# Kernel optimization log

Hardware: AMD Instinct MI355X
Metric: run time of the kernel (lower is better)

Reference implementation:

```python
import jax, jax.numpy as jnp
import numpy as np

NUM_HEADS = 16
LN_EPS = 1e-5


def _transpose_qkv(X, num_heads):
    # Faithful to the repo's (buggy) transpose_qkv:
    # (B,S,D) -> (B,S,H,D/H) -> permute (B,H,S,D/H) -> reshape (B,S,D)
    B, S, D = X.shape
    X = X.reshape(B, S, num_heads, D // num_heads)
    X = jnp.transpose(X, (0, 2, 1, 3))
    return X.reshape(B, S, D)


def _layer_norm(x, w, b):
    mu = jnp.mean(x, axis=-1, keepdims=True)
    var = jnp.var(x, axis=-1, keepdims=True)
    return (x - mu) * jax.lax.rsqrt(var + LN_EPS) * w + b


def setup_inputs() -> dict:
    key = jax.random.key(0)
    ks = jax.random.split(key, 4)
    B, S, D = 4, 2048, 1024
    scale = 1.0 / np.sqrt(D)
    return {
        "src": jax.random.normal(ks[0], (B, S, D), dtype=jnp.float32),
        "W_q": jax.random.normal(ks[1], (D, D), dtype=jnp.float32) * scale,
        "W_k": jax.random.normal(ks[2], (D, D), dtype=jnp.float32) * scale,
        "W_v": jax.random.normal(ks[3], (D, D), dtype=jnp.float32) * scale,
        "ln1_w": jnp.ones((D,), dtype=jnp.float32),
        "ln1_b": jnp.zeros((D,), dtype=jnp.float32),
        "ln2_w": jnp.ones((D,), dtype=jnp.float32),
        "ln2_b": jnp.zeros((D,), dtype=jnp.float32),
    }


def reference(src, W_q, W_k, W_v, ln1_w, ln1_b, ln2_w, ln2_b):
    # W_* stored as (in, out): y = x @ W  (equivalent to torch Linear, bias=False)
    q = _transpose_qkv(src @ W_q, NUM_HEADS)  # (B,S,D)
    k = _transpose_qkv(src @ W_k, NUM_HEADS)
    v = _transpose_qkv(src @ W_v, NUM_HEADS)
    d = q.shape[-1]  # note: full hidden dim, per the buggy transpose_qkv
    scores = jnp.einsum("bqd,bkd->bqk", q, k) / jnp.sqrt(jnp.float32(d))
    a = jax.nn.softmax(scores, axis=-1)          # (B,S,S) attention weights
    att = jnp.einsum("bqk,bkd->bqd", a, v)       # (B,S,D)
    src2 = _layer_norm(att, ln1_w, ln1_b)        # norm1
    X = _layer_norm(src + src2, ln2_w, ln2_b)    # AddNorm (dropout=0 in eval)
    return (X, a)
```

## Files before the change

### kernel.cpp

```cpp
#include <hip/hip_runtime.h>

typedef _Float16 f16;
typedef __attribute__((ext_vector_type(2))) _Float16 f16x2;
typedef __attribute__((ext_vector_type(4))) _Float16 f16x4;
typedef __attribute__((ext_vector_type(8))) _Float16 f16x8;
typedef __attribute__((ext_vector_type(4))) float f32x4;

#define D_MODEL 1024
#define SEQ 2048
#define NBATCH 4
#define NROWS (NBATCH * SEQ)

__device__ __forceinline__ void gload16(const void* g, void* l) {
  __builtin_amdgcn_global_load_lds(
      (__attribute__((address_space(1))) void*)(void*)g,
      (__attribute__((address_space(3))) void*)l, 16, 0, 0);
}

#define BARF                                   \
  do {                                         \
    asm volatile("" ::: "memory");             \
    __builtin_amdgcn_s_barrier();              \
    asm volatile("" ::: "memory");             \
  } while (0)
#define PRIO1 __builtin_amdgcn_s_setprio(1)
#define PRIO0 __builtin_amdgcn_s_setprio(0)

template <int BN>
__device__ __forceinline__ void gemm8_core(
    const f16* aP0, const f16* aP1, const f16* aP2, const f16* aP3,
    const f16* bP0, const f16* bP1, const f16* bP2, const f16* bP3,
    int stepA, int stepB, int NT, f16* lds, f32x4* acc)
{
  constexpr int NJ = BN / 128;
  constexpr int NACC = 2 * NJ;
  constexpr int SLOT = 16384 + BN * 64;
  const int t = threadIdx.x, l = t & 63;
  const int w = t >> 6, wm = w >> 2, wn = w & 3;
  const int fr = l & 15, g0 = l >> 4;

  int aof[2][4][2], bof[2][NJ][2];
#pragma unroll
  for (int mh = 0; mh < 2; ++mh)
#pragma unroll
    for (int mi = 0; mi < 4; ++mi)
#pragma unroll
      for (int kh = 0; kh < 2; ++kh) {
        const int ra = wm * 128 + mh * 64 + mi * 16 + fr;
        aof[mh][mi][kh] = ra * 64 + (((g0 + kh * 4) ^ (ra & 7)) << 3);
      }
#pragma unroll
  for (int nh = 0; nh < 2; ++nh)
#pragma unroll
    for (int j = 0; j < NJ; ++j)
#pragma unroll
      for (int kh = 0; kh < 2; ++kh) {
        const int rb = (BN == 256) ? (wn * 64 + fr * 4 + nh * 2 + j)
                                   : (wn * 32 + fr * 2 + nh);
        bof[nh][j][kh] = rb * 64 + (((g0 + kh * 4) ^ ((rb >> 2) & 7)) << 3);
      }
#pragma unroll
  for (int i = 0; i < 8 * NACC; ++i) acc[i] = f32x4{0.f, 0.f, 0.f, 0.f};

  f16x8 fa[4][2];
  f16x8 fb[2][NJ][2];

#define STAGE_A(SL)                                  \
  {                                                  \
    f16* d = lds + (SL) * SLOT + t * 8;              \
    gload16(aP0, d);                                 \
    gload16(aP1, d + 4096);                          \
    gload16(aP2, d + 8192);                          \
    gload16(aP3, d + 12288);                         \
  }
#define STAGE_B(SL)                                  \
  {                                                  \
    f16* d = lds + (SL) * SLOT + 16384 + t * 8;      \
    gload16(bP0, d);                                 \
    gload16(bP1, d + 4096);                          \
    if constexpr (BN == 256) {                       \
      gload16(bP2, d + 8192);                        \
      gload16(bP3, d + 12288);                       \
    }                                                \
  }
#define ADVA { aP0 += stepA; aP1 += stepA; aP2 += stepA; aP3 += stepA; }
#define ADVB                                         \
  {                                                  \
    bP0 += stepB; bP1 += stepB;                      \
    if constexpr (BN == 256) { bP2 += stepB; bP3 += stepB; } \
  }
#define VMC                                                        \
  if constexpr (BN == 256) {                                       \
    asm volatile("s_waitcnt vmcnt(4)" ::: "memory");               \
  } else {                                                         \
    asm volatile("s_waitcnt vmcnt(2)" ::: "memory");               \
  }
#define LOAD_A(MH)                                   \
  _Pragma("unroll") for (int mi = 0; mi < 4; ++mi)   \
  _Pragma("unroll") for (int kh = 0; kh < 2; ++kh)   \
      fa[mi][kh] = *(const f16x8*)(LA + aof[MH][mi][kh]);
#define LOAD_B(NH)                                   \
  _Pragma("unroll") for (int j = 0; j < NJ; ++j)     \
  _Pragma("unroll") for (int kh = 0; kh < 2; ++kh)   \
      fb[NH][j][kh] = *(const f16x8*)(LBp + bof[NH][j][kh]);
#define MFMA_BLK(MH, NH)                                                    \
  _Pragma("unroll") for (int mi = 0; mi < 4; ++mi)                          \
  _Pragma("unroll") for (int j = 0; j < NJ; ++j)                            \
  _Pragma("unroll") for (int kh = 0; kh < 2; ++kh)                          \
      acc[((MH)*4 + mi) * NACC + (NH)*NJ + j] =                             \
          __builtin_amdgcn_mfma_f32_16x16x32_f16(                           \
              fa[mi][kh], fb[NH][j][kh],                                    \
              acc[((MH)*4 + mi) * NACC + (NH)*NJ + j], 0, 0, 0);

  (void)bP2; (void)bP3;
  STAGE_A(0); ADVA;
  STAGE_B(0); ADVB;
  STAGE_B(1); ADVB;
  VMC;
  BARF;

  for (int kt = 0; kt < NT; ++kt) {
    const int sl = kt & 1;
    const f16* LA = lds + sl * SLOT;
    const f16* LBp = LA + 16384;
    STAGE_A(sl ^ 1);
    if (kt + 2 < NT) ADVA;
    LOAD_A(0); LOAD_B(0); LOAD_B(1);
    PRIO1; MFMA_BLK(0, 0); MFMA_BLK(0, 1); PRIO0;
    BARF;
    LOAD_A(1);
    STAGE_B(sl);
    if (kt + 3 < NT) ADVB;
    VMC;
    PRIO1; MFMA_BLK(1, 0); MFMA_BLK(1, 1); PRIO0;
    BARF;
  }
#undef STAGE_A
#undef STAGE_B
#undef ADVA
#undef ADVB
#undef VMC
#undef LOAD_A
#undef LOAD_B
#undef MFMA_BLK
}

__global__ __launch_bounds__(512, 2) void k_qkv3(
    const f16* __restrict__ srch, const f16* __restrict__ wt,
    f16* __restrict__ qp, f16* __restrict__ kp, f16* __restrict__ vp)
{
  __shared__ f16 lds[2 * (16384 + 128 * 64)];
  const int t = threadIdx.x, l = t & 63;
  const int w = t >> 6, wm = w >> 2, wn = w & 3;
  const int fr = l & 15, g0 = l >> 4, c = t & 7;
  const int z = blockIdx.y >> 3, cb = blockIdx.y & 7;
  const f16 *aP[4], *bP[2];
#pragma unroll
  for (int i = 0; i < 4; ++i) {
    const int rl = i * 64 + (t >> 3);
    aP[i] = srch + (size_t)(blockIdx.x * 256 + rl) * 1024 + ((c ^ (rl & 7)) << 3);
  }
#pragma unroll
  for (int i = 0; i < 2; ++i) {
    const int rl = i * 64 + (t >> 3);
    bP[i] = wt + ((size_t)z << 20) + (size_t)(cb * 128 + rl) * 1024 +
            ((c ^ ((rl >> 2) & 7)) << 3);
  }
  f32x4 acc[16];
  gemm8_core<128>(aP[0], aP[1], aP[2], aP[3], bP[0], bP[1], bP[0], bP[0],
                  64, 64, 16, lds, acc);
  f16* dst = (z == 0) ? qp : (z == 1 ? kp : vp);
  const int col = cb * 128 + wn * 32 + fr * 2;
#pragma unroll
  for (int mi = 0; mi < 8; ++mi)
#pragma unroll
    for (int q = 0; q < 4; ++q) {
      const int row = blockIdx.x * 256 + wm * 128 + mi * 16 + g0 * 4 + q;
      f16x2 o = {(f16)acc[mi * 2 + 0][q], (f16)acc[mi * 2 + 1][q]};
      *(f16x2*)(dst + (size_t)row * 1024 + col) = o;
    }
}

__global__ __launch_bounds__(512, 2) void k_scores(
    const f16* __restrict__ qp, const f16* __restrict__ kp,
    f16* __restrict__ abf, float* __restrict__ sums)
{
  __shared__ f16 lds[2 * (16384 + 256 * 64)];
  const int t = threadIdx.x, l = t & 63;
  const int w = t >> 6, wm = w >> 2, wn = w & 3;
  const int fr = l & 15, g0 = l >> 4, c = t & 7;
  const int id = blockIdx.x;
  const int wg = ((id & 7) << 5) + (id >> 3);
  const int b = wg >> 6, by = (wg >> 3) & 7, bx = wg & 7;
  const f16* qb = qp + ((size_t)b << 21);
  const f16* kb = kp + ((size_t)b << 21);
  const f16 *aP[4], *bP[4];
#pragma unroll
  for (int i = 0; i < 4; ++i) {
    const int rl = i * 64 + (t >> 3);
    const int spA = bx * 256 + rl;
    aP[i] = qb + (size_t)((spA & 127) << 4) * 1024 + ((spA >> 7) << 6) +
            ((c ^ (rl & 7)) << 3);
    const int spB = by * 256 + rl;
    bP[i] = kb + (size_t)((spB & 127) << 4) * 1024 + ((spB >> 7) << 6) +
            ((c ^ ((rl >> 2) & 7)) << 3);
  }
  f32x4 acc[32];
  gemm8_core<256>(aP[0], aP[1], aP[2], aP[3], bP[0], bP[1], bP[2], bP[3],
                  1024, 1024, 16, lds, acc);
  f16* Cb = abf + ((size_t)b << 22);
  float* sums_b = sums + (b << 11);
  const int col = by * 256 + wn * 64 + fr * 4;
#pragma unroll
  for (int mi = 0; mi < 8; ++mi)
#pragma unroll
    for (int q = 0; q < 4; ++q) {
      const int row = bx * 256 + wm * 128 + mi * 16 + g0 * 4 + q;
      float e0 = __expf(acc[mi * 4 + 0][q] * 0.03125f);
      float e1 = __expf(acc[mi * 4 + 1][q] * 0.03125f);
      float e2 = __expf(acc[mi * 4 + 2][q] * 0.03125f);
      float e3 = __expf(acc[mi * 4 + 3][q] * 0.03125f);
      f16x4 o = {(f16)e0, (f16)e1, (f16)e2, (f16)e3};
      *(f16x4*)(Cb + (size_t)row * 2048 + col) = o;
      float p = e0 + e1 + e2 + e3;
      p += __shfl_xor(p, 1);
      p += __shfl_xor(p, 2);
      p += __shfl_xor(p, 4);
      p += __shfl_xor(p, 8);
      if (fr == 0) atomicAdd(&sums_b[row], p);
    }
}

__global__ __launch_bounds__(512, 2) void k_att(
    const f16* __restrict__ abf, const f16* __restrict__ vtT,
    const float* __restrict__ sums, f16* __restrict__ attb,
    float* __restrict__ Aout)
{
  __shared__ f16 lds[2 * (16384 + 128 * 64)];
  const int t = threadIdx.x, l = t & 63;
  const int w = t >> 6, wm = w >> 2, wn = w & 3;
  const int fr = l & 15, g0 = l >> 4, c = t & 7;
  const int id = blockIdx.x;
  const int wg = ((id & 7) << 5) + (id >> 3);
  const int b = wg >> 6, by = (wg >> 3) & 7, bx = wg & 7;
  const f16* ab = abf + ((size_t)b << 22);
  const f16* vb = vtT + ((size_t)b << 21);
  const f16 *aP[4], *bP[2];
#pragma unroll
  for (int i = 0; i < 4; ++i) {
    const int rl = i * 64 + (t >> 3);
    aP[i] = ab + (size_t)(bx * 256 + rl) * 2048 + ((c ^ (rl & 7)) << 3);
  }
#pragma unroll
  for (int i = 0; i < 2; ++i) {
    const int rl = i * 64 + (t >> 3);
    bP[i] = vb + (size_t)(by * 128 + rl) * 2048 +
            ((c ^ ((rl >> 2) & 7)) << 3);
  }
  f32x4 acc[16];
  gemm8_core<128>(aP[0], aP[1], aP[2], aP[3], bP[0], bP[1], bP[0], bP[0],
                  64, 64, 32, lds, acc);
  const float* sums_b = sums + (b << 11);
  f16* Cb = attb + ((size_t)b << 21);
  const int col = by * 128 + wn * 32 + fr * 2;
#pragma unroll
  for (int mi = 0; mi < 8; ++mi)
#pragma unroll
    for (int q = 0; q < 4; ++q) {
      const int row = bx * 256 + wm * 128 + mi * 16 + g0 * 4 + q;
      const float is = 1.0f / sums_b[row];
      f16x2 o = {(f16)(acc[mi * 2 + 0][q] * is), (f16)(acc[mi * 2 + 1][q] * is)};
      *(f16x2*)(Cb + (size_t)row * 1024 + col) = o;
    }
  float* Ab = Aout + ((size_t)b << 22);
#pragma unroll
  for (int i = 0; i < 16; ++i) {
    const int idx = t + i * 512;
    const int rr = idx >> 5;
    const int cg = (idx & 31) * 8;
    const int grow = bx * 256 + rr;
    const float is = 1.0f / sums_b[grow];
    f16x8 ev = *(const f16x8*)(ab + (size_t)grow * 2048 + by * 256 + cg);
    float4 o0 = {(float)ev[0] * is, (float)ev[1] * is,
                 (float)ev[2] * is, (float)ev[3] * is};
    float4 o1 = {(float)ev[4] * is, (float)ev[5] * is,
                 (float)ev[6] * is, (float)ev[7] * is};
    float* dst = Ab + (size_t)grow * 2048 + by * 256 + cg;
    *(float4*)dst = o0;
    *(float4*)(dst + 4) = o1;
  }
}

__global__ __launch_bounds__(256) void k_prep(
    const float* __restrict__ src, const float* __restrict__ w0,
    const float* __restrict__ w1, const float* __restrict__ w2,
    f16* __restrict__ srch, f16* __restrict__ wt)
{
  const int b = blockIdx.x, t = threadIdx.x;
  if (b < 4096) {
    const size_t i = (size_t)b * 256 + t;
    const float4* p = (const float4*)src;
    float4 v0 = p[2 * i], v1 = p[2 * i + 1];
    f16x8 o;
    o[0] = (f16)v0.x; o[1] = (f16)v0.y; o[2] = (f16)v0.z; o[3] = (f16)v0.w;
    o[4] = (f16)v1.x; o[5] = (f16)v1.y; o[6] = (f16)v1.z; o[7] = (f16)v1.w;
    *(f16x8*)(srch + 8 * i) = o;
    return;
  }
  const int id = b - 4096;
  const int z = id >> 8, rem = id & 255;
  const int bx = rem & 15, by = rem >> 4;
  const float* in = (z == 0) ? w0 : (z == 1 ? w1 : w2);
  f16* o = wt + ((size_t)z << 20);
  __shared__ f16 tile[64][65];
  const int rr = t >> 4, c4 = (t & 15) * 4;
  const int r0 = bx * 64, c0 = by * 64;
#pragma unroll
  for (int i = 0; i < 4; ++i) {
    float4 f = *(const float4*)(in + (size_t)(r0 + rr + 16 * i) * 1024 + c0 + c4);
    tile[rr + 16 * i][c4 + 0] = (f16)f.x;
    tile[rr + 16 * i][c4 + 1] = (f16)f.y;
    tile[rr + 16 * i][c4 + 2] = (f16)f.z;
    tile[rr + 16 * i][c4 + 3] = (f16)f.w;
  }
  __syncthreads();
#pragma unroll
  for (int i = 0; i < 4; ++i) {
    const int n = c0 + rr + 16 * i;
    f16* dst = o + (size_t)n * 1024 + r0 + c4;
    dst[0] = tile[c4 + 0][rr + 16 * i];
    dst[1] = tile[c4 + 1][rr + 16 * i];
    dst[2] = tile[c4 + 2][rr + 16 * i];
    dst[3] = tile[c4 + 3][rr + 16 * i];
  }
}

__global__ __launch_bounds__(256) void k_scrT(const f16* __restrict__ vp,
                                              f16* __restrict__ vtT,
                                              float* __restrict__ sums)
{
  const int t = threadIdx.x;
  if (blockIdx.x == 2048) {
    f32x4 z = {0.f, 0.f, 0.f, 0.f};
#pragma unroll
    for (int i = 0; i < 8; ++i)
      *(f32x4*)(sums + (size_t)(t * 8 + i * 2048) * 4 / 4 + 0) = z,
      ((f32x4*)sums)[t + i * 256] = z;
    return;
  }
  __shared__ f16 tile[64][68];
  const int id = blockIdx.x;
  const int sx = id & 31, sy = (id >> 5) & 15, bz = id >> 9;
  const int sp0 = sx * 64, dp0 = sy * 64;
  const int d6 = dp0 >> 6;
  const int jb = (sp0 >> 7) << 6;
  const int sbase = sp0 & 127;
  const f16* srcv = vp + ((size_t)bz << 21);
  f16* dstv = vtT + ((size_t)bz << 21);
#pragma unroll
  for (int p = 0; p < 2; ++p) {
    const int u = p * 32 + (t >> 3);
    const int s = ((sbase + u) << 4) | d6;
    const int cc = (t & 7) << 3;
    f16x8 v = *(const f16x8*)(srcv + (size_t)s * 1024 + jb + cc);
    *(f16x4*)&tile[u][cc]     = f16x4{v[0], v[1], v[2], v[3]};
    *(f16x4*)&tile[u][cc + 4] = f16x4{v[4], v[5], v[6], v[7]};
  }
  __syncthreads();
#pragma unroll
  for (int p = 0; p < 2; ++p) {
    const int cc = p * 32 + (t >> 3);
    const int v0 = (t & 7) << 3;
    f16x8 o;
#pragma unroll
    for (int j = 0; j < 8; ++j) o[j] = tile[v0 + j][cc];
    *(f16x8*)(dstv + (size_t)(dp0 + cc) * 2048 + sp0 + v0) = o;
  }
}

__global__ __launch_bounds__(256) void k_ln(
    const f16* __restrict__ attb, const float* __restrict__ src,
    const float* __restrict__ w1, const float* __restrict__ b1,
    const float* __restrict__ w2, const float* __restrict__ b2,
    float* __restrict__ out)
{
  const size_t base = (size_t)blockIdx.x * 1024;
  const int t = threadIdx.x, lane = t & 63, w = t >> 6;
  f16x4 a4 = ((const f16x4*)(attb + base))[t];
  float ax = (float)a4[0], ay = (float)a4[1], az = (float)a4[2], aw = (float)a4[3];
  float s = ax + ay + az + aw;
  float s2 = ax * ax + ay * ay + az * az + aw * aw;
#pragma unroll
  for (int off = 1; off < 64; off <<= 1) {
    s += __shfl_xor(s, off);
    s2 += __shfl_xor(s2, off);
  }
  __shared__ float red[16];
  if (lane == 0) { red[w] = s; red[4 + w] = s2; }
  __syncthreads();
  s = red[0] + red[1] + red[2] + red[3];
  s2 = red[4] + red[5] + red[6] + red[7];
  float mu = s * (1.0f / 1024.0f);
  float var = s2 * (1.0f / 1024.0f) - mu * mu;
  float rs = rsqrtf(var + 1e-5f);
  float4 W1 = ((const float4*)w1)[t], B1 = ((const float4*)b1)[t];
  float4 sv = ((const float4*)(src + base))[t];
  float y0 = sv.x + (ax - mu) * rs * W1.x + B1.x;
  float y1 = sv.y + (ay - mu) * rs * W1.y + B1.y;
  float y2 = sv.z + (az - mu) * rs * W1.z + B1.z;
  float y3 = sv.w + (aw - mu) * rs * W1.w + B1.w;
  s = y0 + y1 + y2 + y3;
  s2 = y0 * y0 + y1 * y1 + y2 * y2 + y3 * y3;
#pragma unroll
  for (int off = 1; off < 64; off <<= 1) {
    s += __shfl_xor(s, off);
    s2 += __shfl_xor(s2, off);
  }
  if (lane == 0) { red[8 + w] = s; red[12 + w] = s2; }
  __syncthreads();
  s = red[8] + red[9] + red[10] + red[11];
  s2 = red[12] + red[13] + red[14] + red[15];
  mu = s * (1.0f / 1024.0f);
  var = s2 * (1.0f / 1024.0f) - mu * mu;
  rs = rsqrtf(var + 1e-5f);
  float4 W2 = ((const float4*)w2)[t], B2 = ((const float4*)b2)[t];
  float4 o;
  o.x = (y0 - mu) * rs * W2.x + B2.x;
  o.y = (y1 - mu) * rs * W2.y + B2.y;
  o.z = (y2 - mu) * rs * W2.z + B2.z;
  o.w = (y3 - mu) * rs * W2.w + B2.w;
  ((float4*)(out + base))[t] = o;
}

extern "C" void kernel_launch(void* const* d_in, const int* in_sizes, int n_in,
                              void* d_out, int out_size, void* d_ws, size_t ws_size,
                              hipStream_t stream) {
  const float* src = (const float*)d_in[0];
  const float* Wq  = (const float*)d_in[1];
  const float* Wk  = (const float*)d_in[2];
  const float* Wv  = (const float*)d_in[3];
  const float* l1w = (const float*)d_in[4];
  const float* l1b = (const float*)d_in[5];
  const float* l2w = (const float*)d_in[6];
  const float* l2b = (const float*)d_in[7];
  float* Xout = (float*)d_out;
  float* Aout = Xout + (size_t)NROWS * D_MODEL;

  char* ws = (char*)d_ws;
  f16* srch = (f16*)ws;
  float* sums = (float*)ws;
  f16* wt   = (f16*)(ws + (16u << 20));
  f16* qp   = (f16*)(ws + (22u << 20));
  f16* kp   = (f16*)(ws + (38u << 20));
  f16* vp   = (f16*)(ws + (54u << 20));
  f16* vtT  = (f16*)(ws + (70u << 20));
  f16* abf  = (f16*)(ws + (86u << 20));
  f16* attb = (f16*)(ws + (118u << 20));

  k_prep<<<4864, 256, 0, stream>>>(src, Wq, Wk, Wv, srch, wt);
  k_qkv3<<<dim3(32, 24), 512, 0, stream>>>(srch, wt, qp, kp, vp);
  k_scrT<<<2049, 256, 0, stream>>>(vp, vtT, sums);
  k_scores<<<256, 512, 0, stream>>>(qp, kp, abf, sums);
  k_att<<<256, 512, 0, stream>>>(abf, vtT, sums, attb, Aout);
  k_ln<<<NROWS, 256, 0, stream>>>(attb, src, l1w, l1b, l2w, l2b, Xout);
}
```

Measured before the change: 193.2 us.

## Inline attention-V GEMM loop and fuse normalized A output writes from LDS fragments

Replaces the generic gemm8_core call in k_att with an inlined double-buffered loop that stages A and V tiles through LDS and interleaves MFMA halves with barriers. The fp32 attention-weight output is now written from the fragments already loaded for the MFMA, by the wn==0 waves when the k-tile falls in this block's column slice. This drops the separate epilogue that re-read the unnormalized fp16 scores from global memory. It also removes a redundant duplicate zeroing store in k_scrT. The cost is more register pressure and store work placed inside the main loop for some waves, which may unbalance them.

```diff
diff --git a/kernel.cpp b/kernel.cpp
--- a/kernel.cpp
+++ b/kernel.cpp
@@ -245,22 +245,132 @@
   const int b = wg >> 6, by = (wg >> 3) & 7, bx = wg & 7;
   const f16* ab = abf + ((size_t)b << 22);
   const f16* vb = vtT + ((size_t)b << 21);
-  const f16 *aP[4], *bP[2];
-#pragma unroll
-  for (int i = 0; i < 4; ++i) {
-    const int rl = i * 64 + (t >> 3);
-    aP[i] = ab + (size_t)(bx * 256 + rl) * 2048 + ((c ^ (rl & 7)) << 3);
-  }
-#pragma unroll
-  for (int i = 0; i < 2; ++i) {
-    const int rl = i * 64 + (t >> 3);
-    bP[i] = vb + (size_t)(by * 128 + rl) * 2048 +
-            ((c ^ ((rl >> 2) & 7)) << 3);
-  }
+  const float* sums_b = sums + (b << 11);
+  float* Ab = Aout + ((size_t)b << 22);
+
+  const f16 *aP0, *aP1, *aP2, *aP3, *bP0, *bP1;
+  {
+    const int rl0 = (t >> 3), rl1 = 64 + rl0, rl2 = 128 + rl0, rl3 = 192 + rl0;
+    aP0 = ab + (size_t)(bx * 256 + rl0) * 2048 + ((c ^ (rl0 & 7)) << 3);
+    aP1 = ab + (size_t)(bx * 256 + rl1) * 2048 + ((c ^ (rl1 & 7)) << 3);
+    aP2 = ab + (size_t)(bx * 256 + rl2) * 2048 + ((c ^ (rl2 & 7)) << 3);
+    aP3 = ab + (size_t)(bx * 256 + rl3) * 2048 + ((c ^ (rl3 & 7)) << 3);
+    bP0 = vb + (size_t)(by * 128 + rl0) * 2048 + ((c ^ ((rl0 >> 2) & 7)) << 3);
+    bP1 = vb + (size_t)(by * 128 + rl1) * 2048 + ((c ^ ((rl1 >> 2) & 7)) << 3);
+  }
+
+  int aof[2][4][2], bof[2][2];
+#pragma unroll
+  for (int mh = 0; mh < 2; ++mh)
+#pragma unroll
+    for (int mi = 0; mi < 4; ++mi)
+#pragma unroll
+      for (int kh = 0; kh < 2; ++kh) {
+        const int ra = wm * 128 + mh * 64 + mi * 16 + fr;
+        aof[mh][mi][kh] = ra * 64 + (((g0 + kh * 4) ^ (ra & 7)) << 3);
+      }
+#pragma unroll
+  for (int nh = 0; nh < 2; ++nh)
+#pragma unroll
+    for (int kh = 0; kh < 2; ++kh) {
+      const int rb = wn * 32 + fr * 2 + nh;
+      bof[nh][kh] = rb * 64 + (((g0 + kh * 4) ^ ((rb >> 2) & 7)) << 3);
+    }
+  float is8[2][4];
+#pragma unroll
+  for (int mh = 0; mh < 2; ++mh)
+#pragma unroll
+    for (int mi = 0; mi < 4; ++mi)
+      is8[mh][mi] = 1.0f / sums_b[bx * 256 + wm * 128 + mh * 64 + mi * 16 + fr];
+
   f32x4 acc[16];
-  gemm8_core<128>(aP[0], aP[1], aP[2], aP[3], bP[0], bP[1], bP[0], bP[0],
-                  64, 64, 32, lds, acc);
-  const float* sums_b = sums + (b << 11);
+#pragma unroll
+  for (int i = 0; i < 16; ++i) acc[i] = f32x4{0.f, 0.f, 0.f, 0.f};
+  f16x8 fa[4][2], fb[2][2];
+  constexpr int SLOT = 16384 + 8192;
+
+#define ASTG(SL)                                     \
+  {                                                  \
+    f16* d = lds + (SL) * SLOT + t * 8;              \
+    gload16(aP0, d);                                 \
+    gload16(aP1, d + 4096);                          \
+    gload16(aP2, d + 8192);                          \
+    gload16(aP3, d + 12288);                         \
+  }
+#define BSTG(SL)                                     \
+  {                                                  \
+    f16* d = lds + (SL) * SLOT + 16384 + t * 8;      \
+    gload16(bP0, d);                                 \
+    gload16(bP1, d + 4096);                          \
+  }
+#define AADV { aP0 += 64; aP1 += 64; aP2 += 64; aP3 += 64; }
+#define BADV { bP0 += 64; bP1 += 64; }
+#define VM2 asm volatile("s_waitcnt vmcnt(2)" ::: "memory")
+#define LDA_(MH)                                     \
+  _Pragma("unroll") for (int mi = 0; mi < 4; ++mi)   \
+  _Pragma("unroll") for (int kh = 0; kh < 2; ++kh)   \
+      fa[mi][kh] = *(const f16x8*)(LA + aof[MH][mi][kh]);
+#define LDB_(NH)                                     \
+  _Pragma("unroll") for (int kh = 0; kh < 2; ++kh)   \
+      fb[NH][kh] = *(const f16x8*)(LBp + bof[NH][kh]);
+#define MFM_(MH, NH)                                                        \
+  _Pragma("unroll") for (int mi = 0; mi < 4; ++mi)                          \
+  _Pragma("unroll") for (int kh = 0; kh < 2; ++kh)                          \
+      acc[((MH)*4 + mi) * 2 + (NH)] =                                       \
+          __builtin_amdgcn_mfma_f32_16x16x32_f16(                           \
+              fa[mi][kh], fb[NH][kh], acc[((MH)*4 + mi) * 2 + (NH)], 0, 0, 0);
+#define AWR(MH)                                                             \
+  if (wn == 0 && (kt >> 2) == by) {                                         \
+    _Pragma("unroll") for (int mi = 0; mi < 4; ++mi)                        \
+    _Pragma("unroll") for (int kh = 0; kh < 2; ++kh) {                      \
+      const int grow = bx * 256 + wm * 128 + (MH) * 64 + mi * 16 + fr;      \
+      const int kc = kt * 64 + (g0 + kh * 4) * 8;                           \
+      const float is = is8[MH][mi];                                         \
+      float* dst = Ab + (size_t)grow * 2048 + kc;                           \
+      f32x4 o0 = {(float)fa[mi][kh][0] * is, (float)fa[mi][kh][1] * is,     \
+                  (float)fa[mi][kh][2] * is, (float)fa[mi][kh][3] * is};    \
+      f32x4 o1 = {(float)fa[mi][kh][4] * is, (float)fa[mi][kh][5] * is,     \
+                  (float)fa[mi][kh][6] * is, (float)fa[mi][kh][7] * is};    \
+      *(f32x4*)dst = o0;                                                    \
+      *(f32x4*)(dst + 4) = o1;                                              \
+    }                                                                       \
+  }
+
+  ASTG(0); AADV;
+  BSTG(0); BADV;
+  BSTG(1); BADV;
+  VM2;
+  BARF;
+
+#pragma unroll 1
+  for (int kt = 0; kt < 32; ++kt) {
+    const int sl = kt & 1;
+    const f16* LA = lds + sl * SLOT;
+    const f16* LBp = LA + 16384;
+    ASTG(sl ^ 1);
+    if (kt + 2 < 32) AADV;
+    LDA_(0); LDB_(0); LDB_(1);
+    PRIO1; MFM_(0, 0); MFM_(0, 1); PRIO0;
+    AWR(0);
+    BARF;
+    LDA_(1);
+    BSTG(sl);
+    if (kt + 3 < 32) BADV;
+    VM2;
+    PRIO1; MFM_(1, 0); MFM_(1, 1); PRIO0;
+    AWR(1);
+    BARF;
+  }
+#undef ASTG
+#undef BSTG
+#undef AADV
+#undef BADV
+#undef VM2
+#undef LDA_
+#undef LDB_
+#undef MFM_
+#undef AWR
+
   f16* Cb = attb + ((size_t)b << 21);
   const int col = by * 128 + wn * 32 + fr * 2;
 #pragma unroll
@@ -272,23 +382,6 @@
       f16x2 o = {(f16)(acc[mi * 2 + 0][q] * is), (f16)(acc[mi * 2 + 1][q] * is)};
       *(f16x2*)(Cb + (size_t)row * 1024 + col) = o;
     }
-  float* Ab = Aout + ((size_t)b << 22);
-#pragma unroll
-  for (int i = 0; i < 16; ++i) {
-    const int idx = t + i * 512;
-    const int rr = idx >> 5;
-    const int cg = (idx & 31) * 8;
-    const int grow = bx * 256 + rr;
-    const float is = 1.0f / sums_b[grow];
-    f16x8 ev = *(const f16x8*)(ab + (size_t)grow * 2048 + by * 256 + cg);
-    float4 o0 = {(float)ev[0] * is, (float)ev[1] * is,
-                 (float)ev[2] * is, (float)ev[3] * is};
-    float4 o1 = {(float)ev[4] * is, (float)ev[5] * is,
-                 (float)ev[6] * is, (float)ev[7] * is};
-    float* dst = Ab + (size_t)grow * 2048 + by * 256 + cg;
-    *(float4*)dst = o0;
-    *(float4*)(dst + 4) = o1;
-  }
 }
 
 __global__ __launch_bounds__(256) void k_prep(
@@ -343,9 +436,7 @@
   if (blockIdx.x == 2048) {
     f32x4 z = {0.f, 0.f, 0.f, 0.f};
 #pragma unroll
-    for (int i = 0; i < 8; ++i)
-      *(f32x4*)(sums + (size_t)(t * 8 + i * 2048) * 4 / 4 + 0) = z,
-      ((f32x4*)sums)[t + i * 256] = z;
+    for (int i = 0; i < 8; ++i) ((f32x4*)sums)[t + i * 256] = z;
     return;
   }
   __shared__ f16 tile[64][68];
```

New measurement: 185.2 us. 1.04x faster.
